# Kernel optimization log

Measured on AMD Instinct MI355X. Metric: run time of the kernel, lower is better.

## Reference

```python
import jax, jax.numpy as jnp
import numpy as np

T, B, E = 2048, 2, 1024
H = 16
D = E // H


def setup_inputs() -> dict:
    key = jax.random.key(0)
    ks = jax.random.split(key, 7)
    s = 1.0 / np.sqrt(E)
    return {
        "query": jax.random.normal(ks[0], (T, B, E), jnp.float32),
        "key": jax.random.normal(ks[1], (T, B, E), jnp.float32),
        "value": jax.random.normal(ks[2], (T, B, E), jnp.float32),
        "in_proj_weight": jax.random.normal(ks[3], (3 * E, E), jnp.float32) * s,
        "in_proj_bias": jax.random.normal(ks[4], (3 * E,), jnp.float32) * 0.02,
        "out_proj_weight": jax.random.normal(ks[5], (E, E), jnp.float32) * s,
        "out_proj_bias": jax.random.normal(ks[6], (E,), jnp.float32) * 0.02,
    }


def reference(query, key, value, in_proj_weight, in_proj_bias, out_proj_weight, out_proj_bias):
    tgt_len, bsz, embed_dim = query.shape
    src_len = key.shape[0]
    head_dim = embed_dim // H
    # packed in-projection (F.linear: x @ W.T + b)
    w_q, w_k, w_v = jnp.split(in_proj_weight, 3, axis=0)
    b_q, b_k, b_v = jnp.split(in_proj_bias, 3, axis=0)
    q = query @ w_q.T + b_q   # [T, B, E]
    k = key @ w_k.T + b_k     # [S, B, E]
    v = value @ w_v.T + b_v   # [S, B, E]
    # [T,B,E] -> [B,H,T,D]
    q = q.reshape(tgt_len, bsz, H, head_dim).transpose(1, 2, 0, 3)
    k = k.reshape(src_len, bsz, H, head_dim).transpose(1, 2, 0, 3)
    v = v.reshape(src_len, bsz, H, head_dim).transpose(1, 2, 0, 3)
    scale = 1.0 / jnp.sqrt(jnp.asarray(head_dim, q.dtype))
    scores = jnp.einsum("bhtd,bhsd->bhts", q, k) * scale  # [B,H,T,S]
    attn_weights = jax.nn.softmax(scores, axis=-1)
    attn = jnp.einsum("bhts,bhsd->bhtd", attn_weights, v)  # [B,H,T,D]
    # [B,H,T,D] -> [T,B,E]
    attn = attn.transpose(2, 0, 1, 3).reshape(tgt_len, bsz, embed_dim)
    attn_output = attn @ out_proj_weight.T + out_proj_bias  # [T,B,E]
    # averaged attention weights over heads (average_attn_weights=True)
    avg_weights = jnp.sum(attn_weights, axis=1) / H  # [B,T,S]
    return attn_output, avg_weights
```

## Files before the change

kernel.cpp:

```cpp
#include <hip/hip_runtime.h>
#include <hip/hip_bf16.h>

typedef float  f32x2  __attribute__((ext_vector_type(2)));
typedef float  f32x4  __attribute__((ext_vector_type(4)));
typedef float  f32x16 __attribute__((ext_vector_type(16)));
typedef __bf16 bf16x8 __attribute__((ext_vector_type(8)));

#define MFMA16(A,B,C) __builtin_amdgcn_mfma_f32_16x16x32_bf16((A),(B),(C),0,0,0)
#define MFMA32(A,B,C) __builtin_amdgcn_mfma_f32_32x32x16_bf16((A),(B),(C),0,0,0)
#define EXP2(x) __builtin_amdgcn_exp2f(x)
#define LOG2(x) __builtin_amdgcn_logf(x)

static constexpr int Tn = 2048, Bn = 2, En = 1024, Hn = 16, Dn = 64;
static constexpr float kQScale = 0.125f * 1.4426950408889634f;

static __device__ __forceinline__ unsigned pack2(float a, float b) {
  union { __bf16 h[2]; unsigned u; } un;
  un.h[0] = (__bf16)a; un.h[1] = (__bf16)b;
  return un.u;
}

__global__ __launch_bounds__(256)
void k_qkv(const float* __restrict__ Xq, const float* __restrict__ Xk,
           const float* __restrict__ Xv, const float* __restrict__ W,
           const float* __restrict__ bias,
           __bf16* __restrict__ q_ws, __bf16* __restrict__ k_ws,
           __bf16* __restrict__ v_ws)
{
  __shared__ bf16x8 Asm[128 * 4];
  __shared__ bf16x8 Bsm[128 * 4];
  const int tid = threadIdx.x;
  const int lane = tid & 63, w = tid >> 6;
  const int wr = w >> 1, wc = w & 1;
  const int ag = lane >> 4, lr = lane & 15;
  const int mBase = blockIdx.x * 128;
  const int oBase = blockIdx.y * 128;
  const int which = blockIdx.y >> 3;
  const float* X  = (which == 0) ? Xq : ((which == 1) ? Xk : Xv);
  const float* Wt = W + (size_t)oBase * En;
  __bf16* dst = (which == 0) ? q_ws : ((which == 1) ? k_ws : v_ws);
  const float oscale = (which == 0) ? kQScale : 1.0f;

  f32x4 acc[4][4];
  #pragma unroll
  for (int i = 0; i < 4; ++i)
    #pragma unroll
    for (int j = 0; j < 4; ++j) { f32x4 z = {0.f, 0.f, 0.f, 0.f}; acc[i][j] = z; }

  for (int kk = 0; kk < En; kk += 32) {
    __syncthreads();
    #pragma unroll
    for (int it = 0; it < 2; ++it) {
      int gi = tid + it * 256;
      int row = gi >> 2, gg = gi & 3;
      const float* pa = X  + (size_t)(mBase + row) * En + kk + gg * 8;
      const float* pb = Wt + (size_t)row * En + kk + gg * 8;
      f32x4 a0 = *reinterpret_cast<const f32x4*>(pa);
      f32x4 a1 = *reinterpret_cast<const f32x4*>(pa + 4);
      f32x4 b0 = *reinterpret_cast<const f32x4*>(pb);
      f32x4 b1 = *reinterpret_cast<const f32x4*>(pb + 4);
      bf16x8 av, bv;
      #pragma unroll
      for (int e = 0; e < 4; ++e) {
        av[e] = (__bf16)a0[e]; av[e + 4] = (__bf16)a1[e];
        bv[e] = (__bf16)b0[e]; bv[e + 4] = (__bf16)b1[e];
      }
      int sg = gg ^ ((row >> 1) & 3);
      Asm[row * 4 + sg] = av;
      Bsm[row * 4 + sg] = bv;
    }
    __syncthreads();
    bf16x8 af[4], bfr[4];
    #pragma unroll
    for (int mb = 0; mb < 4; ++mb) {
      int row = wr * 64 + mb * 16 + lr;
      af[mb] = Asm[row * 4 + (ag ^ ((row >> 1) & 3))];
    }
    #pragma unroll
    for (int nb = 0; nb < 4; ++nb) {
      int row = wc * 64 + nb * 16 + lr;
      bfr[nb] = Bsm[row * 4 + (ag ^ ((row >> 1) & 3))];
    }
    #pragma unroll
    for (int mb = 0; mb < 4; ++mb)
      #pragma unroll
      for (int nb = 0; nb < 4; ++nb)
        acc[mb][nb] = MFMA16(af[mb], bfr[nb], acc[mb][nb]);
  }

  #pragma unroll
  for (int nb = 0; nb < 4; ++nb) {
    int oG = oBase + wc * 64 + nb * 16 + lr;
    float bv = bias[oG];
    int oS = oG & (En - 1);
    int h = oS >> 6, d = oS & 63;
    #pragma unroll
    for (int mb = 0; mb < 4; ++mb)
      #pragma unroll
      for (int r = 0; r < 4; ++r) {
        int i = mBase + wr * 64 + mb * 16 + ag * 4 + r;
        int t = i >> 1, b2 = i & 1;
        dst[(((size_t)(b2 * Hn + h)) * Tn + t) * Dn + d] =
            (__bf16)((acc[mb][nb][r] + bv) * oscale);
      }
  }
}

__global__ __launch_bounds__(256)
void k_transpose_v(const __bf16* __restrict__ v_ws, __bf16* __restrict__ vt_ws)
{
  __shared__ __bf16 tile[64][72];
  const int bh = blockIdx.x >> 5;
  const int tt = blockIdx.x & 31;
  const int tid = threadIdx.x;
  const __bf16* src = v_ws + ((size_t)bh * Tn + tt * 64) * Dn;
  #pragma unroll
  for (int it = 0; it < 2; ++it) {
    int gi = tid + it * 256;
    int row = gi >> 3, gg = gi & 7;
    *reinterpret_cast<bf16x8*>(&tile[row][gg * 8]) =
        *reinterpret_cast<const bf16x8*>(src + row * Dn + gg * 8);
  }
  __syncthreads();
  __bf16* dst = vt_ws + (size_t)bh * Dn * Tn + tt * 64;
  #pragma unroll
  for (int it = 0; it < 2; ++it) {
    int gi = tid + it * 256;
    int drow = gi >> 3, tg = gi & 7;
    bf16x8 vv;
    #pragma unroll
    for (int e = 0; e < 8; ++e) vv[e] = tile[tg * 8 + e][drow];
    *reinterpret_cast<bf16x8*>(dst + (size_t)drow * Tn + tg * 8) = vv;
  }
}

__global__ __launch_bounds__(256, 2)
void k_flash(const __bf16* __restrict__ q_ws, const __bf16* __restrict__ k_ws,
             const __bf16* __restrict__ vt_ws, __bf16* __restrict__ ctx,
             float* __restrict__ stats)
{
  __shared__ __align__(16) char k_sm[8192];
  __shared__ __align__(16) char v_sm[8192];
  __shared__ __align__(16) float es_sm[4][32];

  const int tid = threadIdx.x;
  const int lane = tid & 63, w = tid >> 6;
  const int tl = lane & 31, hi = lane >> 5;
  const int bh = blockIdx.x >> 4;
  const int qt = blockIdx.x & 15;
  const int t0w = qt * 128 + w * 32;

  const __bf16* kbase  = k_ws + (size_t)bh * Tn * Dn;
  const __bf16* vtbase = vt_ws + (size_t)bh * Dn * Tn;

  bf16x8 qf[4];
  {
    const __bf16* qrow = q_ws + ((size_t)bh * Tn + t0w + tl) * Dn + hi * 8;
    #pragma unroll
    for (int c = 0; c < 4; ++c)
      qf[c] = *reinterpret_cast<const bf16x8*>(qrow + c * 16);
  }

  f32x16 accO0, accO1;
  #pragma unroll
  for (int i = 0; i < 16; ++i) { accO0[i] = 0.f; accO1[i] = 0.f; }
  float m_run = -INFINITY, l_run = 0.f;

  const int r0 = tid >> 3, s0 = tid & 7;
  const int ldso = ((s0 ^ (r0 & 7)) << 4);
  const int ko0 = r0 * 128 + ldso, ko1 = ko0 + 32 * 128;

  bf16x8 rk0 = *(const bf16x8*)(kbase + r0 * 64 + s0 * 8);
  bf16x8 rk1 = *(const bf16x8*)(kbase + (r0 + 32) * 64 + s0 * 8);
  bf16x8 rv0 = *(const bf16x8*)(vtbase + (size_t)r0 * Tn + s0 * 8);
  bf16x8 rv1 = *(const bf16x8*)(vtbase + (size_t)(r0 + 32) * Tn + s0 * 8);

  for (int st = 0; st < 32; ++st) {
    __syncthreads();
    *(bf16x8*)(k_sm + ko0) = rk0;
    *(bf16x8*)(k_sm + ko1) = rk1;
    *(bf16x8*)(v_sm + ko0) = rv0;
    *(bf16x8*)(v_sm + ko1) = rv1;
    __syncthreads();
    if (st + 1 < 32) {
      const __bf16* kn = kbase + (size_t)(st + 1) * 64 * Dn;
      const __bf16* vn = vtbase + (st + 1) * 64;
      rk0 = *(const bf16x8*)(kn + r0 * 64 + s0 * 8);
      rk1 = *(const bf16x8*)(kn + (r0 + 32) * 64 + s0 * 8);
      rv0 = *(const bf16x8*)(vn + (size_t)r0 * Tn + s0 * 8);
      rv1 = *(const bf16x8*)(vn + (size_t)(r0 + 32) * Tn + s0 * 8);
    }

    f32x16 sc0, sc1;
    #pragma unroll
    for (int i = 0; i < 16; ++i) { sc0[i] = 0.f; sc1[i] = 0.f; }
    const char* kr0 = k_sm + tl * 128;
    const char* kr1 = k_sm + (32 + tl) * 128;
    #pragma unroll
    for (int c = 0; c < 4; ++c) {
      const int off = (((2 * c + hi) ^ (tl & 7)) << 4);
      sc0 = MFMA32(*(const bf16x8*)(kr0 + off), qf[c], sc0);
      sc1 = MFMA32(*(const bf16x8*)(kr1 + off), qf[c], sc1);
    }

    float mx[8];
    #pragma unroll
    for (int i = 0; i < 8; ++i)
      mx[i] = fmaxf(fmaxf(sc0[i], sc0[i + 8]), fmaxf(sc1[i], sc1[i + 8]));
    float tm = fmaxf(fmaxf(fmaxf(mx[0], mx[1]), fmaxf(mx[2], mx[3])),
                     fmaxf(fmaxf(mx[4], mx[5]), fmaxf(mx[6], mx[7])));
    tm = fmaxf(tm, __shfl_xor(tm, 32, 64));
    const float mn = fmaxf(m_run, tm);
    const float es = EXP2(m_run - mn);
    m_run = mn;
    #pragma unroll
    for (int i = 0; i < 16; ++i) {
      sc0[i] = EXP2(sc0[i] - mn);
      sc1[i] = EXP2(sc1[i] - mn);
    }
    float p0s = 0.f, p1s = 0.f, p2s = 0.f, p3s = 0.f;
    #pragma unroll
    for (int i = 0; i < 16; i += 4) {
      p0s += sc0[i]     + sc1[i];
      p1s += sc0[i + 1] + sc1[i + 1];
      p2s += sc0[i + 2] + sc1[i + 2];
      p3s += sc0[i + 3] + sc1[i + 3];
    }
    float rs = (p0s + p1s) + (p2s + p3s);
    rs += __shfl_xor(rs, 32, 64);
    l_run = l_run * es + rs;

    es_sm[w][tl] = es;
    f32x4 esr[4];
    #pragma unroll
    for (int q = 0; q < 4; ++q)
      esr[q] = *(const f32x4*)&es_sm[w][8 * q + 4 * hi];
    #pragma unroll
    for (int q = 0; q < 4; ++q)
      #pragma unroll
      for (int rr = 0; rr < 4; ++rr) {
        accO0[q * 4 + rr] *= esr[q][rr];
        accO1[q * 4 + rr] *= esr[q][rr];
      }

    unsigned wA0[4], wB0[4], wA1[4], wB1[4];
    #pragma unroll
    for (int g = 0; g < 4; ++g) {
      wA0[g] = pack2(sc0[4 * g],     sc0[4 * g + 1]);
      wB0[g] = pack2(sc0[4 * g + 2], sc0[4 * g + 3]);
      wA1[g] = pack2(sc1[4 * g],     sc1[4 * g + 1]);
      wB1[g] = pack2(sc1[4 * g + 2], sc1[4 * g + 3]);
    }
    bf16x8 pa[2][2];
    #pragma unroll
    for (int sb = 0; sb < 2; ++sb) {
      const unsigned* WA = sb ? wA1 : wA0;
      const unsigned* WB = sb ? wB1 : wB0;
      #pragma unroll
      for (int c = 0; c < 2; ++c) {
        unsigned a0 = WA[2 * c], a1 = WA[2 * c + 1];
        unsigned b0 = WB[2 * c], b1 = WB[2 * c + 1];
        unsigned xa0 = __shfl_xor(a0, 32, 64);
        unsigned xa1 = __shfl_xor(a1, 32, 64);
        unsigned xb0 = __shfl_xor(b0, 32, 64);
        unsigned xb1 = __shfl_xor(b1, 32, 64);
        union { unsigned u[4]; bf16x8 v; } uu;
        uu.u[0] = hi ? xa1 : a0;
        uu.u[1] = hi ? xb1 : b0;
        uu.u[2] = hi ? a1 : xa0;
        uu.u[3] = hi ? b1 : xb0;
        pa[sb][c] = uu.v;
      }
    }

    const char* vr0 = v_sm + tl * 128;
    const char* vr1 = v_sm + (32 + tl) * 128;
    #pragma unroll
    for (int sb = 0; sb < 2; ++sb)
      #pragma unroll
      for (int c = 0; c < 2; ++c) {
        const int off = (((sb * 4 + c * 2 + hi) ^ (tl & 7)) << 4);
        accO0 = MFMA32(pa[sb][c], *(const bf16x8*)(vr0 + off), accO0);
        accO1 = MFMA32(pa[sb][c], *(const bf16x8*)(vr1 + off), accO1);
      }
  }

  const float linv = 1.0f / l_run;
  es_sm[w][tl] = linv;
  f32x4 lr[4];
  #pragma unroll
  for (int q = 0; q < 4; ++q)
    lr[q] = *(const f32x4*)&es_sm[w][8 * q + 4 * hi];
  const int b2 = bh >> 4, h = bh & 15;
  #pragma unroll
  for (int q = 0; q < 4; ++q)
    #pragma unroll
    for (int rr = 0; rr < 4; ++rr) {
      const int t = t0w + 8 * q + 4 * hi + rr;
      __bf16* cp = ctx + ((size_t)t * Bn + b2) * En + h * 64 + tl;
      cp[0]  = (__bf16)(accO0[q * 4 + rr] * lr[q][rr]);
      cp[32] = (__bf16)(accO1[q * 4 + rr] * lr[q][rr]);
    }
  if (hi == 0) {
    const int t = t0w + tl;
    f32x2 stv; stv[0] = m_run; stv[1] = l_run;
    *reinterpret_cast<f32x2*>(&stats[((size_t)bh * Tn + t) * 2]) = stv;
  }
}

__global__ __launch_bounds__(256)
void k_avgw(const __bf16* __restrict__ q_ws, const __bf16* __restrict__ k_ws,
            const float* __restrict__ stats, float* __restrict__ avg_out)
{
  __shared__ __align__(16) char q_sm[8192];
  __shared__ __align__(16) char k_sm[8192];
  __shared__ __align__(16) float adj_sm[16][64];

  const int tid = threadIdx.x;
  const int lane = tid & 63, w = tid >> 6;
  const int tl = lane & 31, hi = lane >> 5;
  const int b2 = blockIdx.x >> 10;
  const int tt = (blockIdx.x >> 5) & 31;
  const int ss = blockIdx.x & 31;
  const int thalf = (w >> 1) * 32, shalf = (w & 1) * 32;

  #pragma unroll
  for (int it = 0; it < 4; ++it) {
    int idx = tid + it * 256;
    int h = idx >> 6, trow = idx & 63;
    f32x2 sv = *(const f32x2*)&stats[(((size_t)(b2 * Hn + h)) * Tn + tt * 64 + trow) * 2];
    adj_sm[h][trow] = sv[0] + LOG2(16.0f * sv[1]);
  }

  const size_t hstride = (size_t)Tn * Dn;
  const __bf16* qb = q_ws + ((size_t)(b2 * Hn) * Tn + tt * 64) * Dn;
  const __bf16* kb = k_ws + ((size_t)(b2 * Hn) * Tn + ss * 64) * Dn;

  const int r0 = tid >> 3, s0 = tid & 7;
  const int ldso = ((s0 ^ (r0 & 7)) << 4);
  const int ko0 = r0 * 128 + ldso, ko1 = ko0 + 32 * 128;

  bf16x8 rq0 = *(const bf16x8*)(qb + r0 * 64 + s0 * 8);
  bf16x8 rq1 = *(const bf16x8*)(qb + (r0 + 32) * 64 + s0 * 8);
  bf16x8 rk0 = *(const bf16x8*)(kb + r0 * 64 + s0 * 8);
  bf16x8 rk1 = *(const bf16x8*)(kb + (r0 + 32) * 64 + s0 * 8);

  f32x16 avg;
  #pragma unroll
  for (int i = 0; i < 16; ++i) avg[i] = 0.f;

  const char* qr = q_sm + (thalf + tl) * 128;
  const char* kr = k_sm + (shalf + tl) * 128;

  for (int h = 0; h < Hn; ++h) {
    __syncthreads();
    *(bf16x8*)(q_sm + ko0) = rq0;
    *(bf16x8*)(q_sm + ko1) = rq1;
    *(bf16x8*)(k_sm + ko0) = rk0;
    *(bf16x8*)(k_sm + ko1) = rk1;
    __syncthreads();
    if (h + 1 < Hn) {
      const __bf16* qn = qb + (size_t)(h + 1) * hstride;
      const __bf16* kn = kb + (size_t)(h + 1) * hstride;
      rq0 = *(const bf16x8*)(qn + r0 * 64 + s0 * 8);
      rq1 = *(const bf16x8*)(qn + (r0 + 32) * 64 + s0 * 8);
      rk0 = *(const bf16x8*)(kn + r0 * 64 + s0 * 8);
      rk1 = *(const bf16x8*)(kn + (r0 + 32) * 64 + s0 * 8);
    }

    f32x16 sc;
    #pragma unroll
    for (int i = 0; i < 16; ++i) sc[i] = 0.f;
    #pragma unroll
    for (int c = 0; c < 4; ++c) {
      const int off = (((2 * c + hi) ^ (tl & 7)) << 4);
      sc = MFMA32(*(const bf16x8*)(qr + off), *(const bf16x8*)(kr + off), sc);
    }

    #pragma unroll
    for (int q = 0; q < 4; ++q) {
      f32x4 ad = *(const f32x4*)&adj_sm[h][thalf + 8 * q + 4 * hi];
      #pragma unroll
      for (int r = 0; r < 4; ++r)
        avg[q * 4 + r] += EXP2(sc[q * 4 + r] - ad[r]);
    }
  }

  #pragma unroll
  for (int q = 0; q < 4; ++q)
    #pragma unroll
    for (int r = 0; r < 4; ++r) {
      int t = tt * 64 + thalf + 8 * q + 4 * hi + r;
      int s = ss * 64 + shalf + tl;
      avg_out[((size_t)(b2 * Tn + t)) * Tn + s] = avg[q * 4 + r];
    }
}

__global__ __launch_bounds__(256)
void k_outproj(const __bf16* __restrict__ ctx, const float* __restrict__ W,
               const float* __restrict__ bias, float* __restrict__ out)
{
  __shared__ bf16x8 Asm[128 * 4];
  __shared__ bf16x8 Bsm[128 * 4];
  const int tid = threadIdx.x;
  const int lane = tid & 63, w = tid >> 6;
  const int wr = w >> 1, wc = w & 1;
  const int ag = lane >> 4, lr = lane & 15;
  const int mBase = blockIdx.x * 128;
  const int oBase = blockIdx.y * 128;

  f32x4 acc[4][4];
  #pragma unroll
  for (int i = 0; i < 4; ++i)
    #pragma unroll
    for (int j = 0; j < 4; ++j) { f32x4 z = {0.f,0.f,0.f,0.f}; acc[i][j] = z; }

  for (int kk = 0; kk < En; kk += 32) {
    __syncthreads();
    #pragma unroll
    for (int it = 0; it < 2; ++it) {
      int gi = tid + it * 256;
      int row = gi >> 2, gg = gi & 3;
      bf16x8 av = *reinterpret_cast<const bf16x8*>(
          ctx + (size_t)(mBase + row) * En + kk + gg * 8);
      const float* pb = W + (size_t)(oBase + row) * En + kk + gg * 8;
      f32x4 b0 = *reinterpret_cast<const f32x4*>(pb);
      f32x4 b1 = *reinterpret_cast<const f32x4*>(pb + 4);
      bf16x8 bv;
      #pragma unroll
      for (int e = 0; e < 4; ++e) { bv[e] = (__bf16)b0[e]; bv[e + 4] = (__bf16)b1[e]; }
      int sg = gg ^ ((row >> 1) & 3);
      Asm[row * 4 + sg] = av;
      Bsm[row * 4 + sg] = bv;
    }
    __syncthreads();
    bf16x8 af[4], bfr[4];
    #pragma unroll
    for (int mb = 0; mb < 4; ++mb) {
      int row = wr * 64 + mb * 16 + lr;
      af[mb] = Asm[row * 4 + (ag ^ ((row >> 1) & 3))];
    }
    #pragma unroll
    for (int nb = 0; nb < 4; ++nb) {
      int row = wc * 64 + nb * 16 + lr;
      bfr[nb] = Bsm[row * 4 + (ag ^ ((row >> 1) & 3))];
    }
    #pragma unroll
    for (int mb = 0; mb < 4; ++mb)
      #pragma unroll
      for (int nb = 0; nb < 4; ++nb)
        acc[mb][nb] = MFMA16(af[mb], bfr[nb], acc[mb][nb]);
  }

  #pragma unroll
  for (int nb = 0; nb < 4; ++nb) {
    int o = oBase + wc * 64 + nb * 16 + lr;
    float bv = bias[o];
    #pragma unroll
    for (int mb = 0; mb < 4; ++mb)
      #pragma unroll
      for (int r = 0; r < 4; ++r) {
        int i = mBase + wr * 64 + mb * 16 + ag * 4 + r;
        out[(size_t)i * En + o] = acc[mb][nb][r] + bv;
      }
  }
}

extern "C" void kernel_launch(void* const* d_in, const int* in_sizes, int n_in,
                              void* d_out, int out_size, void* d_ws, size_t ws_size,
                              hipStream_t stream)
{
  (void)in_sizes; (void)n_in; (void)out_size; (void)ws_size;
  const float* query = (const float*)d_in[0];
  const float* key   = (const float*)d_in[1];
  const float* value = (const float*)d_in[2];
  const float* in_w  = (const float*)d_in[3];
  const float* in_b  = (const float*)d_in[4];
  const float* out_w = (const float*)d_in[5];
  const float* out_b = (const float*)d_in[6];

  float* attn_out = (float*)d_out;
  float* avg_out  = (float*)d_out + (size_t)Tn * Bn * En;

  char* ws = (char*)d_ws;
  __bf16* q_ws  = (__bf16*)(ws);
  __bf16* k_ws  = (__bf16*)(ws + (8u  << 20));
  __bf16* v_ws  = (__bf16*)(ws + (16u << 20));
  __bf16* vt_ws = (__bf16*)(ws + (24u << 20));
  __bf16* ctx   = (__bf16*)(ws + (32u << 20));
  float*  stats = (float*)(ws + (40u << 20));

  k_qkv<<<dim3(32, 24), 256, 0, stream>>>(query, key, value, in_w, in_b,
                                          q_ws, k_ws, v_ws);
  k_transpose_v<<<1024, 256, 0, stream>>>(v_ws, vt_ws);
  k_flash<<<512, 256, 0, stream>>>(q_ws, k_ws, vt_ws, ctx, stats);
  k_avgw<<<2048, 256, 0, stream>>>(q_ws, k_ws, stats, avg_out);
  k_outproj<<<dim3(32, 8), 256, 0, stream>>>(ctx, out_w, out_b, attn_out);
}
```

Before: 207.7 us.

## Pre-convert inputs and weights to bf16 and stage GEMM tiles via direct global-to-LDS loads

Adds a conversion kernel that casts the query, key and value activations and both weight matrices from fp32 to bf16 into workspace buffers. The QKV and output-projection GEMMs then load bf16 tiles straight into LDS with global_load_lds, replacing the register round trip, in-loop conversion and swizzled LDS stores. The extra kernel adds a full read and write pass over the inputs and weights. The LDS layout is now unswizzled k-group-major, which may cause bank conflicts on the fragment reads. Workspace regions are reused as conversion scratch, relying on later kernels overwriting them.

```diff
diff --git a/kernel.cpp b/kernel.cpp
--- a/kernel.cpp
+++ b/kernel.cpp
@@ -20,15 +20,47 @@
   return un.u;
 }
 
+static __device__ __forceinline__ void gload_lds16(const void* g, void* l) {
+  __builtin_amdgcn_global_load_lds(
+      (const __attribute__((address_space(1))) void*)g,
+      (__attribute__((address_space(3))) void*)l, 16, 0, 0);
+}
+
 __global__ __launch_bounds__(256)
-void k_qkv(const float* __restrict__ Xq, const float* __restrict__ Xk,
-           const float* __restrict__ Xv, const float* __restrict__ W,
+void k_cvt(const float* __restrict__ q, const float* __restrict__ k,
+           const float* __restrict__ v, const float* __restrict__ w3,
+           const float* __restrict__ wo,
+           __bf16* __restrict__ qb, __bf16* __restrict__ kb,
+           __bf16* __restrict__ vb, __bf16* __restrict__ w3b,
+           __bf16* __restrict__ wob)
+{
+  const size_t g = (size_t)blockIdx.x * 256 + threadIdx.x;
+  const float* src;
+  __bf16* dst;
+  size_t off;
+  if (g < 524288)        { src = q;  dst = qb;  off = g; }
+  else if (g < 1048576)  { src = k;  dst = kb;  off = g - 524288; }
+  else if (g < 1572864)  { src = v;  dst = vb;  off = g - 1048576; }
+  else if (g < 1966080)  { src = w3; dst = w3b; off = g - 1572864; }
+  else                   { src = wo; dst = wob; off = g - 1966080; }
+  const float* p = src + off * 8;
+  f32x4 a = *reinterpret_cast<const f32x4*>(p);
+  f32x4 b = *reinterpret_cast<const f32x4*>(p + 4);
+  bf16x8 o;
+  #pragma unroll
+  for (int e = 0; e < 4; ++e) { o[e] = (__bf16)a[e]; o[e + 4] = (__bf16)b[e]; }
+  *reinterpret_cast<bf16x8*>(dst + off * 8) = o;
+}
+
+__global__ __launch_bounds__(256)
+void k_qkv(const __bf16* __restrict__ Xq, const __bf16* __restrict__ Xk,
+           const __bf16* __restrict__ Xv, const __bf16* __restrict__ W,
            const float* __restrict__ bias,
            __bf16* __restrict__ q_ws, __bf16* __restrict__ k_ws,
            __bf16* __restrict__ v_ws)
 {
-  __shared__ bf16x8 Asm[128 * 4];
-  __shared__ bf16x8 Bsm[128 * 4];
+  __shared__ __align__(16) char a_lds[8192];
+  __shared__ __align__(16) char b_lds[8192];
   const int tid = threadIdx.x;
   const int lane = tid & 63, w = tid >> 6;
   const int wr = w >> 1, wc = w & 1;
@@ -36,11 +68,23 @@
   const int mBase = blockIdx.x * 128;
   const int oBase = blockIdx.y * 128;
   const int which = blockIdx.y >> 3;
-  const float* X  = (which == 0) ? Xq : ((which == 1) ? Xk : Xv);
-  const float* Wt = W + (size_t)oBase * En;
+  const __bf16* X  = (which == 0) ? Xq : ((which == 1) ? Xk : Xv);
+  const __bf16* Wt = W + (size_t)oBase * En;
   __bf16* dst = (which == 0) ? q_ws : ((which == 1) ? k_ws : v_ws);
   const float oscale = (which == 0) ? kQScale : 1.0f;
 
+  const int g0 = w >> 1, h0 = w & 1;
+  const int gA = w;
+  char* laA0 = a_lds + gA * 2048;
+  char* laA1 = a_lds + gA * 2048 + 1024;
+  char* lbA0 = b_lds + gA * 2048;
+  char* lbA1 = b_lds + gA * 2048 + 1024;
+  const __bf16* pa0 = X  + (size_t)(mBase + lane) * En + gA * 8;
+  const __bf16* pa1 = X  + (size_t)(mBase + 64 + lane) * En + gA * 8;
+  const __bf16* pb0 = Wt + (size_t)(lane) * En + gA * 8;
+  const __bf16* pb1 = Wt + (size_t)(64 + lane) * En + gA * 8;
+  (void)g0; (void)h0;
+
   f32x4 acc[4][4];
   #pragma unroll
   for (int i = 0; i < 4; ++i)
@@ -49,38 +93,18 @@
 
   for (int kk = 0; kk < En; kk += 32) {
     __syncthreads();
-    #pragma unroll
-    for (int it = 0; it < 2; ++it) {
-      int gi = tid + it * 256;
-      int row = gi >> 2, gg = gi & 3;
-      const float* pa = X  + (size_t)(mBase + row) * En + kk + gg * 8;
-      const float* pb = Wt + (size_t)row * En + kk + gg * 8;
-      f32x4 a0 = *reinterpret_cast<const f32x4*>(pa);
-      f32x4 a1 = *reinterpret_cast<const f32x4*>(pa + 4);
-      f32x4 b0 = *reinterpret_cast<const f32x4*>(pb);
-      f32x4 b1 = *reinterpret_cast<const f32x4*>(pb + 4);
-      bf16x8 av, bv;
-      #pragma unroll
-      for (int e = 0; e < 4; ++e) {
-        av[e] = (__bf16)a0[e]; av[e + 4] = (__bf16)a1[e];
-        bv[e] = (__bf16)b0[e]; bv[e + 4] = (__bf16)b1[e];
-      }
-      int sg = gg ^ ((row >> 1) & 3);
-      Asm[row * 4 + sg] = av;
-      Bsm[row * 4 + sg] = bv;
-    }
+    gload_lds16(pa0 + kk, laA0);
+    gload_lds16(pa1 + kk, laA1);
+    gload_lds16(pb0 + kk, lbA0);
+    gload_lds16(pb1 + kk, lbA1);
     __syncthreads();
     bf16x8 af[4], bfr[4];
     #pragma unroll
-    for (int mb = 0; mb < 4; ++mb) {
-      int row = wr * 64 + mb * 16 + lr;
-      af[mb] = Asm[row * 4 + (ag ^ ((row >> 1) & 3))];
-    }
-    #pragma unroll
-    for (int nb = 0; nb < 4; ++nb) {
-      int row = wc * 64 + nb * 16 + lr;
-      bfr[nb] = Bsm[row * 4 + (ag ^ ((row >> 1) & 3))];
-    }
+    for (int mb = 0; mb < 4; ++mb)
+      af[mb] = *(const bf16x8*)(a_lds + ag * 2048 + (wr * 64 + mb * 16 + lr) * 16);
+    #pragma unroll
+    for (int nb = 0; nb < 4; ++nb)
+      bfr[nb] = *(const bf16x8*)(b_lds + ag * 2048 + (wc * 64 + nb * 16 + lr) * 16);
     #pragma unroll
     for (int mb = 0; mb < 4; ++mb)
       #pragma unroll
@@ -397,17 +421,28 @@
 }
 
 __global__ __launch_bounds__(256)
-void k_outproj(const __bf16* __restrict__ ctx, const float* __restrict__ W,
+void k_outproj(const __bf16* __restrict__ ctx, const __bf16* __restrict__ W,
                const float* __restrict__ bias, float* __restrict__ out)
 {
-  __shared__ bf16x8 Asm[128 * 4];
-  __shared__ bf16x8 Bsm[128 * 4];
+  __shared__ __align__(16) char a_lds[8192];
+  __shared__ __align__(16) char b_lds[8192];
   const int tid = threadIdx.x;
   const int lane = tid & 63, w = tid >> 6;
   const int wr = w >> 1, wc = w & 1;
   const int ag = lane >> 4, lr = lane & 15;
   const int mBase = blockIdx.x * 128;
   const int oBase = blockIdx.y * 128;
+  const __bf16* Wt = W + (size_t)oBase * En;
+
+  const int gA = w;
+  char* laA0 = a_lds + gA * 2048;
+  char* laA1 = a_lds + gA * 2048 + 1024;
+  char* lbA0 = b_lds + gA * 2048;
+  char* lbA1 = b_lds + gA * 2048 + 1024;
+  const __bf16* pa0 = ctx + (size_t)(mBase + lane) * En + gA * 8;
+  const __bf16* pa1 = ctx + (size_t)(mBase + 64 + lane) * En + gA * 8;
+  const __bf16* pb0 = Wt + (size_t)(lane) * En + gA * 8;
+  const __bf16* pb1 = Wt + (size_t)(64 + lane) * En + gA * 8;
 
   f32x4 acc[4][4];
   #pragma unroll
@@ -417,34 +452,18 @@
 
   for (int kk = 0; kk < En; kk += 32) {
     __syncthreads();
-    #pragma unroll
-    for (int it = 0; it < 2; ++it) {
-      int gi = tid + it * 256;
-      int row = gi >> 2, gg = gi & 3;
-      bf16x8 av = *reinterpret_cast<const bf16x8*>(
-          ctx + (size_t)(mBase + row) * En + kk + gg * 8);
-      const float* pb = W + (size_t)(oBase + row) * En + kk + gg * 8;
-      f32x4 b0 = *reinterpret_cast<const f32x4*>(pb);
-      f32x4 b1 = *reinterpret_cast<const f32x4*>(pb + 4);
-      bf16x8 bv;
-      #pragma unroll
-      for (int e = 0; e < 4; ++e) { bv[e] = (__bf16)b0[e]; bv[e + 4] = (__bf16)b1[e]; }
-      int sg = gg ^ ((row >> 1) & 3);
-      Asm[row * 4 + sg] = av;
-      Bsm[row * 4 + sg] = bv;
-    }
+    gload_lds16(pa0 + kk, laA0);
+    gload_lds16(pa1 + kk, laA1);
+    gload_lds16(pb0 + kk, lbA0);
+    gload_lds16(pb1 + kk, lbA1);
     __syncthreads();
     bf16x8 af[4], bfr[4];
     #pragma unroll
-    for (int mb = 0; mb < 4; ++mb) {
-      int row = wr * 64 + mb * 16 + lr;
-      af[mb] = Asm[row * 4 + (ag ^ ((row >> 1) & 3))];
-    }
-    #pragma unroll
-    for (int nb = 0; nb < 4; ++nb) {
-      int row = wc * 64 + nb * 16 + lr;
-      bfr[nb] = Bsm[row * 4 + (ag ^ ((row >> 1) & 3))];
-    }
+    for (int mb = 0; mb < 4; ++mb)
+      af[mb] = *(const bf16x8*)(a_lds + ag * 2048 + (wr * 64 + mb * 16 + lr) * 16);
+    #pragma unroll
+    for (int nb = 0; nb < 4; ++nb)
+      bfr[nb] = *(const bf16x8*)(b_lds + ag * 2048 + (wc * 64 + nb * 16 + lr) * 16);
     #pragma unroll
     for (int mb = 0; mb < 4; ++mb)
       #pragma unroll
@@ -483,17 +502,25 @@
   float* avg_out  = (float*)d_out + (size_t)Tn * Bn * En;
 
   char* ws = (char*)d_ws;
+  const size_t MB = 1u << 20;
   __bf16* q_ws  = (__bf16*)(ws);
-  __bf16* k_ws  = (__bf16*)(ws + (8u  << 20));
-  __bf16* v_ws  = (__bf16*)(ws + (16u << 20));
-  __bf16* vt_ws = (__bf16*)(ws + (24u << 20));
-  __bf16* ctx   = (__bf16*)(ws + (32u << 20));
-  float*  stats = (float*)(ws + (40u << 20));
-
-  k_qkv<<<dim3(32, 24), 256, 0, stream>>>(query, key, value, in_w, in_b,
+  __bf16* k_ws  = (__bf16*)(ws + 8 * MB);
+  __bf16* v_ws  = (__bf16*)(ws + 16 * MB);
+  __bf16* vt_ws = (__bf16*)(ws + 24 * MB);
+  __bf16* ctx   = (__bf16*)(ws + 32 * MB);
+  float*  stats = (float*)(ws + 40 * MB);
+  __bf16* xq_bf = vt_ws;
+  __bf16* xk_bf = ctx;
+  __bf16* xv_bf = (__bf16*)(ws + 40 * MB + 512 * 1024);
+  __bf16* w3_bf = (__bf16*)(ws + 48 * MB + 512 * 1024);
+  __bf16* wo_bf = (__bf16*)(ws + 54 * MB + 512 * 1024);
+
+  k_cvt<<<8192, 256, 0, stream>>>(query, key, value, in_w, out_w,
+                                  xq_bf, xk_bf, xv_bf, w3_bf, wo_bf);
+  k_qkv<<<dim3(32, 24), 256, 0, stream>>>(xq_bf, xk_bf, xv_bf, w3_bf, in_b,
                                           q_ws, k_ws, v_ws);
   k_transpose_v<<<1024, 256, 0, stream>>>(v_ws, vt_ws);
   k_flash<<<512, 256, 0, stream>>>(q_ws, k_ws, vt_ws, ctx, stats);
   k_avgw<<<2048, 256, 0, stream>>>(q_ws, k_ws, stats, avg_out);
-  k_outproj<<<dim3(32, 8), 256, 0, stream>>>(ctx, out_w, out_b, attn_out);
-}
+  k_outproj<<<dim3(32, 8), 256, 0, stream>>>(ctx, wo_bf, out_b, attn_out);
+}
```

Result: slower. 215.0 us (+3.5%).
